# Optimization experiments

Measured on AMD Instinct MI355X. Metric: run time of the kernel, lower is better.

The kernel has to match this reference:

```python
import jax, jax.numpy as jnp
import numpy as np

B, S, D, H = 2, 2048, 1024, 16
HD = D // H  # 64
MASK_VAL = -10000.0


def setup_inputs() -> dict:
    key = jax.random.key(0)
    ks = jax.random.split(key, 8)
    sc = 0.02
    q_features = jax.random.normal(ks[0], (B, S, D), jnp.float32)
    kv_features = jax.random.normal(ks[1], (B, S, D), jnp.float32)
    # causal mask, broadcastable (1,1,S,S)
    mask = jnp.tril(jnp.ones((S, S), jnp.bool_))[None, None]
    Wq = jax.random.normal(ks[2], (D, D), jnp.float32) * sc
    bq = jnp.zeros((D,), jnp.float32)
    Wkv = jax.random.normal(ks[3], (D, 2 * D), jnp.float32) * sc
    bkv = jnp.zeros((2 * D,), jnp.float32)
    Wp = jax.random.normal(ks[4], (D, D), jnp.float32) * sc
    bp = jnp.zeros((D,), jnp.float32)
    return {"q_features": q_features, "kv_features": kv_features, "mask": mask,
            "Wq": Wq, "bq": bq, "Wkv": Wkv, "bkv": bkv, "Wp": Wp, "bp": bp}


def _split_heads(t):
    # (B,S,D) -> (B,H,S,HD)
    return t.reshape(B, S, H, HD).transpose(0, 2, 1, 3)


def reference(q_features, kv_features, mask, Wq, bq, Wkv, bkv, Wp, bp):
    query = q_features @ Wq + bq            # (B,S,D)
    kv = kv_features @ Wkv + bkv            # (B,S,2D)
    key, value = jnp.split(kv, 2, axis=-1)
    q = _split_heads(query)                 # (B,H,S,HD)
    k = _split_heads(key)
    v = _split_heads(value)
    scores = jnp.einsum('bhqd,bhkd->bhqk', q, k) / jnp.sqrt(jnp.float32(HD))
    scores = jnp.where(mask, scores, jnp.asarray(MASK_VAL, scores.dtype))
    attn = jax.nn.softmax(scores, axis=-1)  # (B,H,S,S)
    out = jnp.einsum('bhqk,bhkd->bhqd', attn, v)
    out = out.transpose(0, 2, 1, 3).reshape(B, S, D)  # merge heads
    return out @ Wp + bp
```

## Files before the change

kernel.cpp:

```cpp
#include <hip/hip_runtime.h>

typedef unsigned short u16;
typedef unsigned int u32;
typedef __attribute__((ext_vector_type(4))) unsigned short us4;
typedef __attribute__((ext_vector_type(8))) unsigned short us8;
typedef __attribute__((ext_vector_type(4))) short s16x4;
typedef __attribute__((ext_vector_type(8))) __bf16 bf16x8;
typedef __attribute__((ext_vector_type(4))) float floatx4;

#define S_ 2048
#define D_ 1024
#define QSC 0.18033688f

__device__ __forceinline__ float b2f(u16 u) {
  unsigned v = ((unsigned)u) << 16;
  return __builtin_bit_cast(float, v);
}
__device__ __forceinline__ u16 f2bf(float f) {
  unsigned u = __builtin_bit_cast(unsigned, f);
  unsigned r = (u + 0x7fffu + ((u >> 16) & 1u)) >> 16;
  return (u16)r;
}
__device__ __forceinline__ u16 f2bf_rhu(float f) {
  return (u16)((__builtin_bit_cast(unsigned, f) + 0x8000u) >> 16);
}

typedef const __attribute__((address_space(1))) u32* gas_t;
typedef __attribute__((address_space(3))) u32* las_t;
__device__ __forceinline__ void gload16(const u16* g, u16* l) {
  __builtin_amdgcn_global_load_lds((gas_t)g, (las_t)l, 16, 0, 0);
}

#define PBAR()                                   \
  {                                              \
    __builtin_amdgcn_sched_barrier(0);           \
    asm volatile("" ::: "memory");               \
    __builtin_amdgcn_s_barrier();                \
    asm volatile("" ::: "memory");               \
    __builtin_amdgcn_sched_barrier(0);           \
  }
#define WAITVM(N) asm volatile("s_waitcnt vmcnt(" #N ")" ::: "memory")

__global__ __launch_bounds__(256) void prep(
    const float* __restrict__ qf, const float* __restrict__ kvf,
    const float* __restrict__ Wq, const float* __restrict__ Wkv,
    const float* __restrict__ Wp, u16* __restrict__ qa, u16* __restrict__ kva,
    u16* __restrict__ Wqt, u16* __restrict__ Wkvt, u16* __restrict__ Wpt) {
  int bid = blockIdx.x, tid = threadIdx.x;
  if (bid < 4096) {
    const float* src = (bid < 2048) ? qf : kvf;
    u16* dst = (bid < 2048) ? qa : kva;
    size_t i = ((size_t)(bid & 2047) * 256 + tid) * 8;
    floatx4 a = *(const floatx4*)(src + i);
    floatx4 b = *(const floatx4*)(src + i + 4);
    us8 r;
#pragma unroll
    for (int j = 0; j < 4; j++) { r[j] = f2bf(a[j]); r[4 + j] = f2bf(b[j]); }
    *(us8*)(dst + i) = r;
  } else {
    int t = bid - 4096;
    const float* src; u16* dst; int R, C;
    if (t < 1024)      { src = Wq;  dst = Wqt;  R = 1024; C = 1024; }
    else if (t < 3072) { t -= 1024; src = Wkv; dst = Wkvt; R = 1024; C = 2048; }
    else               { t -= 3072; src = Wp;  dst = Wpt;  R = 1024; C = 1024; }
    int bx = t % (C >> 5), by = t / (C >> 5);
    __shared__ u16 tile[32][33];
    int tx = tid & 31, ty = tid >> 5;
    int x = bx * 32 + tx;
    for (int i = ty; i < 32; i += 8)
      tile[i][tx] = f2bf(src[(size_t)(by * 32 + i) * C + x]);
    __syncthreads();
    int r = tid >> 3, c4 = tid & 7;
    us4 v;
#pragma unroll
    for (int j = 0; j < 4; j++) v[j] = tile[c4 * 4 + j][r];
    *(us4*)&dst[(size_t)(bx * 32 + r) * R + by * 32 + c4 * 4] = v;
  }
}

template <int MODE>
__device__ __forceinline__ void gemm256(
    const u16* __restrict__ A, const u16* __restrict__ Bt,
    const float* __restrict__ bias, void* __restrict__ C0,
    u16* __restrict__ C1, int N, int m0, int n0, u16* smem, float cscale) {
  int tid = threadIdx.x;
  int w = tid >> 6, lane = tid & 63;
  int quad = lane >> 4, l16 = lane & 15;
  int wr = w >> 2, wc = w & 3;

  int srow = w * 32 + (lane >> 2);
  int gchunk = ((lane & 3) ^ ((lane >> 3) & 3)) << 3;
  const u16* Asrc = A + (size_t)(m0 + srow) * 1024 + gchunk;
  const u16* Bsrc = Bt + (size_t)(n0 + srow) * 1024 + gchunk;
  u16* Adst = smem + w * 1024;
  u16* Bdst = smem + 32768 + w * 1024;

  int swz = (quad ^ ((l16 >> 1) & 3)) << 3;
  int aoff = (wr * 128 + l16) * 32 + swz;
  int boff = 32768 + (wc * 64 + l16) * 32 + swz;

  floatx4 acc[8][4] = {};

#define STG(t)                                                 \
  {                                                            \
    int s_ = (t) & 3;                                          \
    gload16(Asrc + (t) * 32, Adst + s_ * 8192);                \
    gload16(Asrc + (t) * 32 + 16384, Adst + s_ * 8192 + 512);  \
    gload16(Bsrc + (t) * 32, Bdst + s_ * 8192);                \
    gload16(Bsrc + (t) * 32 + 16384, Bdst + s_ * 8192 + 512);  \
  }

  STG(0); STG(1); STG(2);
  WAITVM(8);
  PBAR();

#pragma unroll 1
  for (int t = 0; t < 32; t++) {
    int so = (t & 3) * 8192;
    bf16x8 af[8], bf[4];
#pragma unroll
    for (int mf = 0; mf < 8; mf++)
      af[mf] = __builtin_bit_cast(bf16x8,
          *(const us8*)&smem[so + aoff + mf * 512]);
#pragma unroll
    for (int nf = 0; nf < 4; nf++)
      bf[nf] = __builtin_bit_cast(bf16x8,
          *(const us8*)&smem[so + boff + nf * 512]);
    if (t < 29) STG(t + 3);
    __builtin_amdgcn_s_setprio(1);
#pragma unroll
    for (int mf = 0; mf < 8; mf++)
#pragma unroll
      for (int nf = 0; nf < 4; nf++)
        acc[mf][nf] = __builtin_amdgcn_mfma_f32_16x16x32_bf16(
            af[mf], bf[nf], acc[mf][nf], 0, 0, 0);
    __builtin_amdgcn_s_setprio(0);
    if (t < 29)      { WAITVM(8); }
    else if (t == 29){ WAITVM(4); }
    else if (t == 30){ WAITVM(0); }
    if (t < 31) PBAR();
  }
#undef STG

#pragma unroll
  for (int mf = 0; mf < 8; mf++) {
#pragma unroll
    for (int nf = 0; nf < 4; nf++) {
      int col = n0 + wc * 64 + nf * 16 + l16;
      int rowq = m0 + wr * 128 + mf * 16 + quad * 4;
      float bv = bias[col];
      if (MODE == 0) {
        u16* o = (u16*)C0;
#pragma unroll
        for (int r = 0; r < 4; r++)
          o[(size_t)(rowq + r) * N + col] = f2bf((acc[mf][nf][r] + bv) * cscale);
      } else {
        if (col < 1024) {
          u16* o = (u16*)C0;
#pragma unroll
          for (int r = 0; r < 4; r++)
            o[(size_t)(rowq + r) * 1024 + col] = f2bf(acc[mf][nf][r] + bv);
        } else {
          int vcol = col - 1024;
          int b = rowq >> 11, s0 = rowq & 2047;
          us4 pv;
#pragma unroll
          for (int r = 0; r < 4; r++) pv[r] = f2bf(acc[mf][nf][r] + bv);
          *(us4*)&C1[((size_t)(b * 1024 + vcol)) * (size_t)S_ + s0] = pv;
        }
      }
    }
  }
}

__global__ __launch_bounds__(512, 2) void gemm_qkv(
    const u16* __restrict__ qa, const u16* __restrict__ kva,
    const u16* __restrict__ Wqt, const u16* __restrict__ Wkvt,
    const float* __restrict__ bq, const float* __restrict__ bkv,
    u16* __restrict__ Qb, u16* __restrict__ Kb, u16* __restrict__ Vt) {
  __shared__ __align__(16) u16 smem[65536];
  int bid = blockIdx.x;
  int work = (bid & 7) * 24 + (bid >> 3);
  if (work < 64) {
    gemm256<0>(qa, Wqt, bq, Qb, nullptr, 1024,
               (work >> 2) * 256, (work & 3) * 256, smem, QSC);
  } else {
    int lb = work - 64;
    gemm256<2>(kva, Wkvt, bkv, Kb, Vt, 2048,
               (lb >> 3) * 256, (lb & 7) * 256, smem, 1.0f);
  }
}

template <int TM, int TN, int MODE>
__device__ __forceinline__ void gemm4w(
    const u16* __restrict__ A, const u16* __restrict__ Bt,
    const float* __restrict__ bias, void* __restrict__ C0,
    u16* __restrict__ C1, int N, int m0, int n0, u16* smem, float cscale) {
  constexpr int MF = TM / 32, NF = TN / 32;
  constexpr int ASZ = TM * 64;
  constexpr int SLOT = (TM + TN) * 64;
  int tid = threadIdx.x;
  int w = tid >> 6, lane = tid & 63;
  int quad = lane >> 4, l16 = lane & 15;
  int wr = w >> 1, wc = w & 1;

  int gch = ((lane & 7) ^ ((lane >> 3) & 7)) << 3;
  const u16* Ag = A + (size_t)(m0 + w * (TM / 4) + (lane >> 3)) * 1024 + gch;
  const u16* Bg = Bt + (size_t)(n0 + w * (TN / 4) + (lane >> 3)) * 1024 + gch;
  u16* Adst = smem + w * (TM / 4) * 64;
  u16* Bdst = smem + ASZ + w * (TN / 4) * 64;

  int ab = (wr * (TM / 2) + l16) * 64;
  int bb = ASZ + (wc * (TN / 2) + l16) * 64;
  int xk0 = (quad ^ (l16 & 7)) << 3;
  int xk1 = ((4 + quad) ^ (l16 & 7)) << 3;

  floatx4 acc[MF][NF] = {};

#define STAGE4(tn, s_)                                                  \
  {                                                                     \
    _Pragma("unroll") for (int i = 0; i < MF; i++)                      \
      gload16(Ag + (size_t)(tn) * 64 + (size_t)i * 8192,                \
              Adst + (s_) * SLOT + i * 512);                            \
    _Pragma("unroll") for (int i = 0; i < NF; i++)                      \
      gload16(Bg + (size_t)(tn) * 64 + (size_t)i * 8192,                \
              Bdst + (s_) * SLOT + i * 512);                            \
  }

#define COMPUTE4(SOFF)                                                  \
  {                                                                     \
    _Pragma("unroll") for (int kk = 0; kk < 2; kk++) {                  \
      int xk = kk ? xk1 : xk0;                                          \
      bf16x8 bfr[NF];                                                   \
      _Pragma("unroll") for (int nf = 0; nf < NF; nf++)                 \
        bfr[nf] = __builtin_bit_cast(bf16x8,                            \
            *(const us8*)&smem[(SOFF) + bb + nf * 1024 + xk]);          \
      _Pragma("unroll") for (int mf = 0; mf < MF; mf++) {               \
        bf16x8 afr = __builtin_bit_cast(bf16x8,                         \
            *(const us8*)&smem[(SOFF) + ab + mf * 1024 + xk]);          \
        _Pragma("unroll") for (int nf = 0; nf < NF; nf++)               \
          acc[mf][nf] = __builtin_amdgcn_mfma_f32_16x16x32_bf16(        \
              afr, bfr[nf], acc[mf][nf], 0, 0, 0);                      \
      }                                                                 \
    }                                                                   \
  }

  STAGE4(0, 0);
  WAITVM(0);
  PBAR();
#pragma unroll 1
  for (int t = 0; t < 16; t += 2) {
    STAGE4(t + 1, 1);
    COMPUTE4(0);
    WAITVM(0);
    PBAR();
    if (t + 2 < 16) STAGE4(t + 2, 0);
    COMPUTE4(SLOT);
    WAITVM(0);
    PBAR();
  }

#undef STAGE4
#undef COMPUTE4

#pragma unroll
  for (int mf = 0; mf < MF; mf++) {
#pragma unroll
    for (int nf = 0; nf < NF; nf++) {
      int col = n0 + wc * (TN / 2) + nf * 16 + l16;
      int rowq = m0 + wr * (TM / 2) + mf * 16 + quad * 4;
      float bv = bias[col];
      if (MODE == 0) {
        u16* o = (u16*)C0;
#pragma unroll
        for (int r = 0; r < 4; r++)
          o[(size_t)(rowq + r) * N + col] = f2bf((acc[mf][nf][r] + bv) * cscale);
      } else if (MODE == 1) {
        float* o = (float*)C0;
#pragma unroll
        for (int r = 0; r < 4; r++)
          o[(size_t)(rowq + r) * N + col] = acc[mf][nf][r] + bv;
      } else {
        if (col < 1024) {
          u16* o = (u16*)C0;
#pragma unroll
          for (int r = 0; r < 4; r++)
            o[(size_t)(rowq + r) * 1024 + col] = f2bf(acc[mf][nf][r] + bv);
        } else {
          int vcol = col - 1024;
          int b = rowq >> 11, s0 = rowq & 2047;
          us4 pv;
#pragma unroll
          for (int r = 0; r < 4; r++) pv[r] = f2bf(acc[mf][nf][r] + bv);
          *(us4*)&C1[((size_t)(b * 1024 + vcol)) * (size_t)S_ + s0] = pv;
        }
      }
    }
  }
}

__global__ __launch_bounds__(256, 3) void gemm_out(
    const u16* __restrict__ AO, const u16* __restrict__ Wpt,
    const float* __restrict__ bp, float* __restrict__ out) {
  __shared__ __align__(16) u16 smem[24576];
  int work = (blockIdx.x & 7) * 64 + (blockIdx.x >> 3);
  gemm4w<128, 64, 1>(AO, Wpt, bp, out, nullptr, 1024,
                     (work >> 4) * 128, (work & 15) * 64, smem, 1.0f);
}

__global__ __launch_bounds__(256) void attn_fwd(
    const u16* __restrict__ Q, const u16* __restrict__ Kb,
    const u16* __restrict__ Vt, u16* __restrict__ O,
    u16* __restrict__ Opart, float* __restrict__ ml) {
  __shared__ __align__(16) u16 sm[16384];
  int tid  = threadIdx.x;
  int w    = tid >> 6, lane = tid & 63;
  int quad = lane >> 4, l16 = lane & 15;
  int bh = blockIdx.x, b = bh >> 4, h = bh & 15;
  int y = blockIdx.y;

  static const signed char yt_[24] = {15,15,7,14,14,13,13,6,12,12,11,11,5,
                                      10,10,9,9,4,8,8,3,2,1,0};
  static const signed char yh_[24] = {0,1,-1,0,1,0,1,-1,0,1,0,1,-1,
                                      0,1,0,1,-1,0,1,-1,-1,-1,-1};
  int t = yt_[y], hh = yh_[y];
  bool split = hh >= 0;
  int kb0, kb1;
  if (split) { kb0 = hh ? (t + 1) : 0; kb1 = hh ? (2 * t + 2) : (t + 1); }
  else       { kb0 = 0; kb1 = 2 * t + 2; }
  int n = kb1 - kb0;

  const size_t row0 = (size_t)b * S_;
  const u16* Kg = Kb + row0 * D_ + h * 64;
  const u16* Vg = Vt + ((size_t)b * 1024 + h * 64) * S_;

  int qlo = t * 128 + w * 32;
  int dkb = qlo >> 6;
  int qgb = (w & 1) * 32;

  const u16* qp = Q + (row0 + qlo + l16) * D_ + h * 64 + quad * 8;
  bf16x8 aq[2][2];
  aq[0][0] = __builtin_bit_cast(bf16x8, *(const us8*)(qp));
  aq[0][1] = __builtin_bit_cast(bf16x8, *(const us8*)(qp + 32));
  aq[1][0] = __builtin_bit_cast(bf16x8, *(const us8*)(qp + (size_t)16 * D_));
  aq[1][1] = __builtin_bit_cast(bf16x8, *(const us8*)(qp + (size_t)16 * D_ + 32));

  floatx4 o_[2][4] = {};
  floatx4 l_acc[2] = {};
  const s16x4 ones4 = {0x3F80, 0x3F80, 0x3F80, 0x3F80};

  int srow = tid >> 3, c8 = tid & 7;
  int woff = srow * 64 + ((c8 ^ (srow & 7)) << 3);
  u16* smK = sm;
  u16* smV = sm + 8192;

  const u16* Kp = Kg + (size_t)(kb0 * 64 + srow) * D_ + c8 * 8;
  const u16* Vp = Vg + (size_t)srow * S_ + kb0 * 64 + c8 * 8;
  us8 pk0 = *(const us8*)Kp, pk1 = *(const us8*)(Kp + (size_t)32 * D_);
  us8 pv0 = *(const us8*)Vp, pv1 = *(const us8*)(Vp + (size_t)32 * S_);
  *(us8*)&smK[woff] = pk0; *(us8*)&smK[woff + 2048] = pk1;
  *(us8*)&smV[woff] = pv0; *(us8*)&smV[woff + 2048] = pv1;
  if (n > 1) {
    Kp += (size_t)64 * D_; Vp += 64;
    pk0 = *(const us8*)Kp; pk1 = *(const us8*)(Kp + (size_t)32 * D_);
    pv0 = *(const us8*)Vp; pv1 = *(const us8*)(Vp + (size_t)32 * S_);
  }
  __syncthreads();

  for (int i = 0; i < n; i++) {
    int cur = i & 1;
    int kb = kb0 + i;
    if (i + 1 < n) {
      int nxt = (cur ^ 1) * 4096;
      *(us8*)&smK[nxt + woff] = pk0; *(us8*)&smK[nxt + woff + 2048] = pk1;
      *(us8*)&smV[nxt + woff] = pv0; *(us8*)&smV[nxt + woff + 2048] = pv1;
      if (i + 2 < n) {
        Kp += (size_t)64 * D_; Vp += 64;
        pk0 = *(const us8*)Kp; pk1 = *(const us8*)(Kp + (size_t)32 * D_);
        pv0 = *(const us8*)Vp; pv1 = *(const us8*)(Vp + (size_t)32 * S_);
      }
    }
    if (kb <= dkb) {
      const u16* Ksb = smK + cur * 4096;
      const u16* Vsb = smV + cur * 4096;

      floatx4 s[2][4] = {};
      __builtin_amdgcn_s_setprio(1);
#pragma unroll
      for (int kk = 0; kk < 2; kk++)
#pragma unroll
        for (int nt = 0; nt < 4; nt++) {
          us8 kf = *(const us8*)&Ksb[(nt * 16 + l16) * 64 +
                                     (((kk * 4 + quad) ^ (l16 & 7)) << 3)];
          bf16x8 kfb = __builtin_bit_cast(bf16x8, kf);
          s[0][nt] = __builtin_amdgcn_mfma_f32_16x16x32_bf16(
              kfb, aq[0][kk], s[0][nt], 0, 0, 0);
          s[1][nt] = __builtin_amdgcn_mfma_f32_16x16x32_bf16(
              kfb, aq[1][kk], s[1][nt], 0, 0, 0);
        }
      __builtin_amdgcn_s_setprio(0);

      if (kb == dkb) {
#pragma unroll
        for (int hf = 0; hf < 2; hf++) {
          int qg = qgb + hf * 16 + l16;
#pragma unroll
          for (int nt = 0; nt < 4; nt++)
#pragma unroll
            for (int r = 0; r < 4; r++)
              if (nt * 16 + quad * 4 + r > qg) s[hf][nt][r] = -1e5f;
        }
      }

      s16x4 pb[2][4];
#pragma unroll
      for (int hf = 0; hf < 2; hf++)
#pragma unroll
        for (int nt = 0; nt < 4; nt++)
#pragma unroll
          for (int r = 0; r < 4; r++)
            pb[hf][nt][r] = (short)f2bf_rhu(__builtin_amdgcn_exp2f(s[hf][nt][r]));

      __builtin_amdgcn_s_setprio(1);
#pragma unroll
      for (int nt = 0; nt < 4; nt++) {
        l_acc[0] = __builtin_amdgcn_mfma_f32_16x16x16bf16_1k(ones4, pb[0][nt], l_acc[0], 0, 0, 0);
        l_acc[1] = __builtin_amdgcn_mfma_f32_16x16x16bf16_1k(ones4, pb[1][nt], l_acc[1], 0, 0, 0);
#pragma unroll
        for (int mt = 0; mt < 4; mt++) {
          int hd = mt * 16 + l16;
          int chunk = nt * 2 + (quad >> 1);
          us4 vf = *(const us4*)&Vsb[hd * 64 + ((chunk ^ (l16 & 7)) << 3) + (quad & 1) * 4];
          s16x4 vb = __builtin_bit_cast(s16x4, vf);
          o_[0][mt] = __builtin_amdgcn_mfma_f32_16x16x16bf16_1k(
              vb, pb[0][nt], o_[0][mt], 0, 0, 0);
          o_[1][mt] = __builtin_amdgcn_mfma_f32_16x16x16bf16_1k(
              vb, pb[1][nt], o_[1][mt], 0, 0, 0);
        }
      }
      __builtin_amdgcn_s_setprio(0);
    }
    __syncthreads();
  }

  if (!split) {
#pragma unroll
    for (int hf = 0; hf < 2; hf++) {
      float rl = __builtin_amdgcn_rcpf(l_acc[hf][0]);
      size_t orow = (row0 + qlo + hf * 16 + l16) * D_ + h * 64;
#pragma unroll
      for (int mt = 0; mt < 4; mt++) {
        us4 ov;
#pragma unroll
        for (int r = 0; r < 4; r++) ov[r] = f2bf(o_[hf][mt][r] * rl);
        *(us4*)&O[orow + mt * 16 + quad * 4] = ov;
      }
    }
  } else {
    int part = (t - 8) * 2 + hh;
    u16* op = Opart + ((size_t)(bh * 16 + part)) * 8192;
#pragma unroll
    for (int hf = 0; hf < 2; hf++) {
      int rloc = w * 32 + hf * 16 + l16;
#pragma unroll
      for (int mt = 0; mt < 4; mt++) {
        us4 ov;
#pragma unroll
        for (int r = 0; r < 4; r++) ov[r] = f2bf(o_[hf][mt][r]);
        *(us4*)&op[rloc * 64 + mt * 16 + quad * 4] = ov;
      }
      if (quad == 0)
        ml[(size_t)(bh * 16 + part) * 128 + rloc] = l_acc[hf][0];
    }
  }
}

__global__ __launch_bounds__(256) void combine(
    const u16* __restrict__ Opart, const float* __restrict__ ml,
    u16* __restrict__ O) {
  int bh = blockIdx.x, b = bh >> 4, h = bh & 15;
  int t = 8 + blockIdx.y;
  int p0 = bh * 16 + (t - 8) * 2;
  const u16* o1 = Opart + (size_t)p0 * 8192;
  const u16* o2 = o1 + 8192;
  int row = threadIdx.x >> 1, ch = (threadIdx.x & 1) * 32;
  float l1 = ml[(size_t)p0 * 128 + row];
  float l2 = ml[(size_t)(p0 + 1) * 128 + row];
  float inv = __builtin_amdgcn_rcpf(l1 + l2);
  size_t orow = ((size_t)b * S_ + t * 128 + row) * D_ + h * 64 + ch;
#pragma unroll
  for (int v = 0; v < 4; v++) {
    us8 x1 = *(const us8*)&o1[row * 64 + ch + v * 8];
    us8 x2 = *(const us8*)&o2[row * 64 + ch + v * 8];
    us8 out;
#pragma unroll
    for (int j = 0; j < 8; j++)
      out[j] = f2bf((b2f(x1[j]) + b2f(x2[j])) * inv);
    *(us8*)&O[orow + v * 8] = out;
  }
}

extern "C" void kernel_launch(void* const* d_in, const int* in_sizes, int n_in,
                              void* d_out, int out_size, void* d_ws, size_t ws_size,
                              hipStream_t stream) {
  const float* qf  = (const float*)d_in[0];
  const float* kvf = (const float*)d_in[1];
  const float* Wq  = (const float*)d_in[3];
  const float* bq  = (const float*)d_in[4];
  const float* Wkv = (const float*)d_in[5];
  const float* bkv = (const float*)d_in[6];
  const float* Wp  = (const float*)d_in[7];
  const float* bp  = (const float*)d_in[8];

  char* ws = (char*)d_ws;
  const size_t MB = 1048576;
  u16*   kva  = (u16*)(ws);
  u16*   AO   = (u16*)(ws);
  u16*   Kbp  = (u16*)(ws + 8 * MB);
  u16*   Vtp  = (u16*)(ws + 16 * MB);
  u16*   Wqt  = (u16*)(ws + 24 * MB);
  float* mlp  = (float*)(ws + 24 * MB);
  u16*   Wkvt = (u16*)(ws + 26 * MB);
  u16*   Wpt  = (u16*)(ws + 30 * MB);
  u16*   qa    = (u16*)d_out;
  u16*   Opart = (u16*)d_out;
  u16*   Qb    = (u16*)d_out + (size_t)4 * 1048576;

  prep<<<8192, 256, 0, stream>>>(qf, kvf, Wq, Wkv, Wp, qa, kva, Wqt, Wkvt, Wpt);
  gemm_qkv<<<192, 512, 0, stream>>>(qa, kva, Wqt, Wkvt, bq, bkv, Qb, Kbp, Vtp);
  attn_fwd<<<dim3(32, 24), 256, 0, stream>>>(Qb, Kbp, Vtp, AO, Opart, mlp);
  combine<<<dim3(32, 8), 256, 0, stream>>>(Opart, mlp, AO);
  gemm_out<<<512, 256, 0, stream>>>(AO, Wpt, bp, (float*)d_out);
}
```

Before: 212.3 us.

## Double attention query tile to 256 rows with 512-thread blocks

Each attention block now handles 256 query rows with 8 waves instead of 128 rows with 4 waves, so every K/V tile loaded into shared memory is reused by twice as many waves. The causal work split table, the partial-output layout and the combine kernel are all rescaled to match. Each thread now loads one K and one V vector per tile instead of two. The grid halves, which lowers parallelism and may make load balance worse across the causal triangle.

```diff
diff --git a/kernel.cpp b/kernel.cpp
--- a/kernel.cpp
+++ b/kernel.cpp
@@ -308,7 +308,7 @@
                      (work >> 4) * 128, (work & 15) * 64, smem, 1.0f);
 }
 
-__global__ __launch_bounds__(256) void attn_fwd(
+__global__ __launch_bounds__(512, 4) void attn_fwd(
     const u16* __restrict__ Q, const u16* __restrict__ Kb,
     const u16* __restrict__ Vt, u16* __restrict__ O,
     u16* __restrict__ Opart, float* __restrict__ ml) {
@@ -319,22 +319,20 @@
   int bh = blockIdx.x, b = bh >> 4, h = bh & 15;
   int y = blockIdx.y;
 
-  static const signed char yt_[24] = {15,15,7,14,14,13,13,6,12,12,11,11,5,
-                                      10,10,9,9,4,8,8,3,2,1,0};
-  static const signed char yh_[24] = {0,1,-1,0,1,0,1,-1,0,1,0,1,-1,
-                                      0,1,0,1,-1,0,1,-1,-1,-1,-1};
+  static const signed char yt_[12] = {7,7,3,6,6,5,5,2,4,4,1,0};
+  static const signed char yh_[12] = {0,1,-1,0,1,0,1,-1,0,1,-1,-1};
   int t = yt_[y], hh = yh_[y];
   bool split = hh >= 0;
   int kb0, kb1;
-  if (split) { kb0 = hh ? (t + 1) : 0; kb1 = hh ? (2 * t + 2) : (t + 1); }
-  else       { kb0 = 0; kb1 = 2 * t + 2; }
+  if (split) { kb0 = hh ? (2 * t + 2) : 0; kb1 = hh ? (4 * t + 4) : (2 * t + 2); }
+  else       { kb0 = 0; kb1 = 4 * t + 4; }
   int n = kb1 - kb0;
 
   const size_t row0 = (size_t)b * S_;
   const u16* Kg = Kb + row0 * D_ + h * 64;
   const u16* Vg = Vt + ((size_t)b * 1024 + h * 64) * S_;
 
-  int qlo = t * 128 + w * 32;
+  int qlo = t * 256 + w * 32;
   int dkb = qlo >> 6;
   int qgb = (w & 1) * 32;
 
@@ -356,14 +354,12 @@
 
   const u16* Kp = Kg + (size_t)(kb0 * 64 + srow) * D_ + c8 * 8;
   const u16* Vp = Vg + (size_t)srow * S_ + kb0 * 64 + c8 * 8;
-  us8 pk0 = *(const us8*)Kp, pk1 = *(const us8*)(Kp + (size_t)32 * D_);
-  us8 pv0 = *(const us8*)Vp, pv1 = *(const us8*)(Vp + (size_t)32 * S_);
-  *(us8*)&smK[woff] = pk0; *(us8*)&smK[woff + 2048] = pk1;
-  *(us8*)&smV[woff] = pv0; *(us8*)&smV[woff + 2048] = pv1;
+  us8 pk = *(const us8*)Kp, pv = *(const us8*)Vp;
+  *(us8*)&smK[woff] = pk;
+  *(us8*)&smV[woff] = pv;
   if (n > 1) {
     Kp += (size_t)64 * D_; Vp += 64;
-    pk0 = *(const us8*)Kp; pk1 = *(const us8*)(Kp + (size_t)32 * D_);
-    pv0 = *(const us8*)Vp; pv1 = *(const us8*)(Vp + (size_t)32 * S_);
+    pk = *(const us8*)Kp; pv = *(const us8*)Vp;
   }
   __syncthreads();
 
@@ -372,12 +368,11 @@
     int kb = kb0 + i;
     if (i + 1 < n) {
       int nxt = (cur ^ 1) * 4096;
-      *(us8*)&smK[nxt + woff] = pk0; *(us8*)&smK[nxt + woff + 2048] = pk1;
-      *(us8*)&smV[nxt + woff] = pv0; *(us8*)&smV[nxt + woff + 2048] = pv1;
+      *(us8*)&smK[nxt + woff] = pk;
+      *(us8*)&smV[nxt + woff] = pv;
       if (i + 2 < n) {
         Kp += (size_t)64 * D_; Vp += 64;
-        pk0 = *(const us8*)Kp; pk1 = *(const us8*)(Kp + (size_t)32 * D_);
-        pv0 = *(const us8*)Vp; pv1 = *(const us8*)(Vp + (size_t)32 * S_);
+        pk = *(const us8*)Kp; pv = *(const us8*)Vp;
       }
     }
     if (kb <= dkb) {
@@ -457,8 +452,8 @@
       }
     }
   } else {
-    int part = (t - 8) * 2 + hh;
-    u16* op = Opart + ((size_t)(bh * 16 + part)) * 8192;
+    int part = (t - 4) * 2 + hh;
+    u16* op = Opart + ((size_t)(bh * 8 + part)) * 16384;
 #pragma unroll
     for (int hf = 0; hf < 2; hf++) {
       int rloc = w * 32 + hf * 16 + l16;
@@ -470,7 +465,7 @@
         *(us4*)&op[rloc * 64 + mt * 16 + quad * 4] = ov;
       }
       if (quad == 0)
-        ml[(size_t)(bh * 16 + part) * 128 + rloc] = l_acc[hf][0];
+        ml[(size_t)(bh * 8 + part) * 256 + rloc] = l_acc[hf][0];
     }
   }
 }
@@ -479,19 +474,19 @@
     const u16* __restrict__ Opart, const float* __restrict__ ml,
     u16* __restrict__ O) {
   int bh = blockIdx.x, b = bh >> 4, h = bh & 15;
-  int t = 8 + blockIdx.y;
-  int p0 = bh * 16 + (t - 8) * 2;
-  const u16* o1 = Opart + (size_t)p0 * 8192;
-  const u16* o2 = o1 + 8192;
-  int row = threadIdx.x >> 1, ch = (threadIdx.x & 1) * 32;
-  float l1 = ml[(size_t)p0 * 128 + row];
-  float l2 = ml[(size_t)(p0 + 1) * 128 + row];
+  int t = 4 + blockIdx.y;
+  int p0 = bh * 8 + (t - 4) * 2;
+  const u16* o1 = Opart + (size_t)p0 * 16384;
+  const u16* o2 = o1 + 16384;
+  int row = threadIdx.x;
+  float l1 = ml[(size_t)p0 * 256 + row];
+  float l2 = ml[(size_t)(p0 + 1) * 256 + row];
   float inv = __builtin_amdgcn_rcpf(l1 + l2);
-  size_t orow = ((size_t)b * S_ + t * 128 + row) * D_ + h * 64 + ch;
-#pragma unroll
-  for (int v = 0; v < 4; v++) {
-    us8 x1 = *(const us8*)&o1[row * 64 + ch + v * 8];
-    us8 x2 = *(const us8*)&o2[row * 64 + ch + v * 8];
+  size_t orow = ((size_t)b * S_ + t * 256 + row) * D_ + h * 64;
+#pragma unroll
+  for (int v = 0; v < 8; v++) {
+    us8 x1 = *(const us8*)&o1[row * 64 + v * 8];
+    us8 x2 = *(const us8*)&o2[row * 64 + v * 8];
     us8 out;
 #pragma unroll
     for (int j = 0; j < 8; j++)
@@ -528,7 +523,7 @@
 
   prep<<<8192, 256, 0, stream>>>(qf, kvf, Wq, Wkv, Wp, qa, kva, Wqt, Wkvt, Wpt);
   gemm_qkv<<<192, 512, 0, stream>>>(qa, kva, Wqt, Wkvt, bq, bkv, Qb, Kbp, Vtp);
-  attn_fwd<<<dim3(32, 24), 256, 0, stream>>>(Qb, Kbp, Vtp, AO, Opart, mlp);
-  combine<<<dim3(32, 8), 256, 0, stream>>>(Opart, mlp, AO);
+  attn_fwd<<<dim3(32, 12), 512, 0, stream>>>(Qb, Kbp, Vtp, AO, Opart, mlp);
+  combine<<<dim3(32, 4), 256, 0, stream>>>(Opart, mlp, AO);
   gemm_out<<<512, 256, 0, stream>>>(AO, Wpt, bp, (float*)d_out);
 }
```

Result: faster. 205.4 us (-3.3%).
